# Kernel tuning notes

Hardware: AMD Instinct MI355X
Metric: run time of the kernel (lower is better)

Reference implementation:

```python
import jax, jax.numpy as jnp
import numpy as np

VOCAB, EMB, HID, SEQ, BATCH, LAYERS = 10000, 512, 1024, 128, 64, 2

def setup_inputs() -> dict:
    key = jax.random.key(0)
    ks = jax.random.split(key, 9)
    k_emb = np.sqrt(1.0 / HID)
    u = lambda k, shape, a: jax.random.uniform(k, shape, jnp.float32, -a, a)
    return {
        "inputs": jax.random.randint(ks[0], (SEQ, BATCH), 0, VOCAB),
        "hidden": jnp.zeros((LAYERS, BATCH, HID), jnp.float32),
        "emb": u(ks[1], (VOCAB, EMB), 0.1),
        "Wx0": u(ks[2], (HID, EMB), k_emb),
        "Wh0": u(ks[3], (HID, HID), k_emb),
        "bh0": u(ks[4], (HID,), k_emb),
        "Wx1": u(ks[5], (HID, HID), k_emb),
        "Wh1": u(ks[6], (HID, HID), k_emb),
        "bh1": u(ks[7], (HID,), k_emb),
        "Wout": u(ks[8], (VOCAB, HID), 0.1),
        "bout": u(jax.random.fold_in(key, 99), (VOCAB,), 0.1),
    }

def reference(inputs, hidden, emb, Wx0, Wh0, bh0, Wx1, Wh1, bh1, Wout, bout):
    # inputs: (S, B) int; hidden: (L, B, H). Dropout is identity (dp_keep_prob=1).
    embd = emb[inputs]  # (S, B, E)

    def step(h, x_t):
        h0 = jnp.tanh(x_t @ Wx0.T + h[0] @ Wh0.T + bh0)   # (B, H)
        h1 = jnp.tanh(h0 @ Wx1.T + h[1] @ Wh1.T + bh1)    # (B, H)
        logits_t = h1 @ Wout.T + bout                      # (B, V)
        return jnp.stack([h0, h1]), logits_t

    hidden_final, logits = jax.lax.scan(step, hidden, embd)
    return logits, hidden_final
```

## Files before the change

### kernel.cpp

```cpp
#include <hip/hip_runtime.h>
#include <hip/hip_bf16.h>


typedef unsigned short u16;
typedef unsigned int   u32;
typedef unsigned long long u64;
typedef __bf16 bf16x8 __attribute__((ext_vector_type(8)));
typedef float  f32x4  __attribute__((ext_vector_type(4)));

__device__ __forceinline__ u16 f2b(float f) {
  __hip_bfloat16 h = __float2bfloat16(f);
  return __builtin_bit_cast(u16, h);
}
__device__ __forceinline__ float b2f(u16 u) {
  return __bfloat162float(__builtin_bit_cast(__hip_bfloat16, u));
}

__device__ __forceinline__ void gload16(const void* g, void* lds) {
  __builtin_amdgcn_global_load_lds(
      (const __attribute__((address_space(1))) u32*)g,
      (__attribute__((address_space(3))) u32*)lds, 16, 0, 0);
}

__device__ __forceinline__ u64 aload64(const u64* p) {
  return __hip_atomic_load(p, __ATOMIC_RELAXED, __HIP_MEMORY_SCOPE_AGENT);
}
__device__ __forceinline__ void astore64(u64* p, u64 v) {
  __hip_atomic_store(p, v, __ATOMIC_RELAXED, __HIP_MEMORY_SCOPE_AGENT);
}
__device__ __forceinline__ int aloadi(const int* p) {
  return __hip_atomic_load(p, __ATOMIC_RELAXED, __HIP_MEMORY_SCOPE_AGENT);
}
__device__ __forceinline__ void astorei(int* p, int v) {
  __hip_atomic_store(p, v, __ATOMIC_RELAXED, __HIP_MEMORY_SCOPE_AGENT);
}
__device__ __forceinline__ int afetchadd(int* p) {
  return __hip_atomic_fetch_add(p, 1, __ATOMIC_RELAXED,
                                __HIP_MEMORY_SCOPE_AGENT);
}

__device__ __forceinline__ void stage16_1024(char* hbuf, const u64* src,
                                             int tid) {
  const int rsub = tid >> 8;
  const int coff = tid & 255;
  u64 tmp[4];
#pragma unroll
  for (int i = 0; i < 4; ++i) {
    int it = i * 4 + rsub;
    tmp[i] = aload64(src + it * 256 + coff);
  }
#pragma unroll
  for (int i = 0; i < 4; ++i) {
    int it = i * 4 + rsub;
    *(u64*)(hbuf + it * 2048 + ((coff * 8) ^ ((it & 7) << 4))) = tmp[i];
  }
}

__device__ __forceinline__ void cvt4(const float* __restrict__ s,
                                     u16* __restrict__ d, int n4,
                                     int gid, int stride) {
  for (int i = gid; i < n4; i += stride) {
    float4 f = ((const float4*)s)[i];
    ushort4 u;
    u.x = f2b(f.x); u.y = f2b(f.y); u.z = f2b(f.z); u.w = f2b(f.w);
    ((ushort4*)d)[i] = u;
  }
}

__global__ __launch_bounds__(256) void prep_kernel(
    const int* __restrict__ inputs, const float* __restrict__ hidden,
    const float* __restrict__ emb,
    const float* __restrict__ Wx0, const float* __restrict__ Wh0,
    const float* __restrict__ Wx1, const float* __restrict__ Wh1,
    const float* __restrict__ Wout,
    u16* Wx0b, u16* Wh0b, u16* Wcat1, u16* Woutb,
    u16* A0b, u16* Hh0, u16* Hh1, int* flags) {
  int gid = blockIdx.x * 256 + threadIdx.x;
  int stride = gridDim.x * 256;
  if (gid < 1024) flags[gid] = 0;
  cvt4(Wx0, Wx0b, 1024 * 512 / 4, gid, stride);
  cvt4(Wh0, Wh0b, 1024 * 1024 / 4, gid, stride);
  cvt4(Wout, Woutb, 10000 * 1024 / 4, gid, stride);
  cvt4(hidden, Hh0, 65536 / 4, gid, stride);
  cvt4(hidden + 65536, Hh1, 65536 / 4, gid, stride);
  for (int i = gid; i < 1024 * 512; i += stride) {
    int row = i >> 9, j = i & 511;
    float4 f = (j < 256) ? ((const float4*)Wx1)[row * 256 + j]
                         : ((const float4*)Wh1)[row * 256 + (j - 256)];
    ushort4 u;
    u.x = f2b(f.x); u.y = f2b(f.y); u.z = f2b(f.z); u.w = f2b(f.w);
    ((ushort4*)Wcat1)[i] = u;
  }
  for (int i = gid; i < 8192 * 128; i += stride) {
    int m = i >> 7, e4 = i & 127;
    int r = inputs[m];
    float4 f = ((const float4*)(emb + (size_t)r * 512))[e4];
    ushort4 u;
    u.x = f2b(f.x); u.y = f2b(f.y); u.z = f2b(f.z); u.w = f2b(f.w);
    ((ushort4*)A0b)[i] = u;
  }
}

__global__ __launch_bounds__(256) void gemm_bt(
    const u16* __restrict__ A, const u16* __restrict__ Bm,
    const float* __restrict__ bias, u16* __restrict__ Cout,
    int M, int N, int K) {
  const int tid = threadIdx.x;
  const int l = tid & 63;
  const int wv = tid >> 6;
  const int MT = M >> 7;
  const int bm = (int)blockIdx.x % MT;
  const int bn = (int)blockIdx.x / MT;
  const int m0 = bm * 128, n0 = bn * 128;

  __shared__ u16 As[128 * 32];
  __shared__ u16 Bs[128 * 32];

  const int fa0 = wv * 1024 + l * 16;
  const int fa1 = (4 + wv) * 1024 + l * 16;
  const int rowA0 = fa0 >> 6, kO0 = (fa0 & 63) >> 1;
  const int rowA1 = fa1 >> 6, kO1 = (fa1 & 63) >> 1;
  const u16* gA0 = A + (size_t)(m0 + rowA0) * K + kO0;
  const u16* gA1 = A + (size_t)(m0 + rowA1) * K + kO1;
  const u16* gB0 = Bm + (size_t)(n0 + rowA0) * K + kO0;
  const u16* gB1 = Bm + (size_t)(n0 + rowA1) * K + kO1;
  u16* lA0 = As + wv * 512;
  u16* lA1 = As + (4 + wv) * 512;
  u16* lB0 = Bs + wv * 512;
  u16* lB1 = Bs + (4 + wv) * 512;

  const int wm = wv >> 1, wn = wv & 1;
  const u16* pA = As + (wm * 64 + (l & 15)) * 32 + (l >> 4) * 8;
  const u16* pB = Bs + (wn * 64 + (l & 15)) * 32 + (l >> 4) * 8;

  f32x4 acc[4][4] = {};

  for (int k0 = 0; k0 < K; k0 += 32) {
    __syncthreads();
    gload16(gA0 + k0, lA0);
    gload16(gA1 + k0, lA1);
    gload16(gB0 + k0, lB0);
    gload16(gB1 + k0, lB1);
    asm volatile("s_waitcnt vmcnt(0)" ::: "memory");
    __syncthreads();
    bf16x8 a[4], b[4];
#pragma unroll
    for (int i = 0; i < 4; ++i) a[i] = *(const bf16x8*)(pA + i * 512);
#pragma unroll
    for (int j = 0; j < 4; ++j) b[j] = *(const bf16x8*)(pB + j * 512);
#pragma unroll
    for (int i = 0; i < 4; ++i)
#pragma unroll
      for (int j = 0; j < 4; ++j)
        acc[i][j] = __builtin_amdgcn_mfma_f32_16x16x32_bf16(a[i], b[j],
                                                            acc[i][j], 0, 0, 0);
  }

#pragma unroll
  for (int j = 0; j < 4; ++j) {
    int cn = n0 + wn * 64 + j * 16 + (l & 15);
    float bv = bias[cn];
#pragma unroll
    for (int i = 0; i < 4; ++i) {
      int rmb = m0 + wm * 64 + i * 16 + ((l >> 4) << 2);
#pragma unroll
      for (int r = 0; r < 4; ++r)
        Cout[(size_t)(rmb + r) * N + cn] = f2b(acc[i][j][r] + bv);
    }
  }
}

__global__ __launch_bounds__(1024, 4) void rnn_fused(
    const u16* __restrict__ X0, const u16* __restrict__ Wh0b,
    const u16* __restrict__ Wcat1, const float* __restrict__ bh1,
    u16* __restrict__ Hh0, u16* __restrict__ Hh1,
    const u16* __restrict__ Woutb, const float* __restrict__ bout,
    float* __restrict__ outL,
    float* __restrict__ hfin0, float* __restrict__ hfin1,
    int* __restrict__ flags) {
  __shared__ __align__(16) char smem[65664];
  const int tid = threadIdx.x;
  const int l = tid & 63;
  const int wv = tid >> 6;

  if (blockIdx.x < 32) {
    char* hbuf = smem;
    float (*red)[16][16] = (float(*)[16][16])(smem + 32768);
    u16* ht = (u16*)(smem + 40960);
    const int wg = (int)blockIdx.x;
    const int bg = wg & 3, cc = wg >> 2;
    const int cw = wv & 7, kw = wv >> 3;
    const int col = cc * 128 + cw * 16 + (l & 15);
    const int row = l & 15;
    const int sw = (row & 7) << 4;
    const int rowoff = row * 2048;
    const int kwbase = kw * 1024 + ((l >> 4) << 4);
    bf16x8 b[16];
    {
      const u16* wp = Wh0b + (size_t)col * 1024 + (kw * 512 + ((l >> 4) * 8));
#pragma unroll
      for (int kt = 0; kt < 16; ++kt) b[kt] = *(const bf16x8*)(wp + kt * 32);
    }
    int* cnt0 = flags + (bg << 4);
    int* done0 = flags + 64 + (bg << 4);

    for (int t = 0; t < 128; ++t) {
      float xv[4];
      if (kw == 0) {
#pragma unroll
        for (int r = 0; r < 4; ++r) {
          int bat = bg * 16 + (l >> 4) * 4 + r;
          xv[r] = b2f(X0[(size_t)(t * 64 + bat) * 1024 + col]);
        }
      }
      stage16_1024(hbuf, (const u64*)(Hh0 + ((size_t)t * 64 + bg * 16) * 1024),
                   tid);
      __syncthreads();
      f32x4 acc = {0.f, 0.f, 0.f, 0.f};
#pragma unroll
      for (int kt = 0; kt < 16; ++kt) {
        bf16x8 av =
            *(const bf16x8*)(hbuf + rowoff + ((kwbase + kt * 64) ^ sw));
        acc = __builtin_amdgcn_mfma_f32_16x16x32_bf16(av, b[kt], acc, 0, 0, 0);
      }
      if (kw == 1) {
#pragma unroll
        for (int r = 0; r < 4; ++r) red[cw][(l >> 4) * 4 + r][l & 15] = acc[r];
      }
      __syncthreads();
      if (kw == 0) {
#pragma unroll
        for (int r = 0; r < 4; ++r) {
          int br = (l >> 4) * 4 + r;
          float v = acc[r] + red[cw][br][l & 15] + xv[r];
          v = tanhf(v);
          ht[br * 128 + cw * 16 + (l & 15)] = f2b(v);
          if (t == 127) hfin0[(bg * 16 + br) * 1024 + col] = v;
        }
      }
      __syncthreads();
      if (tid < 512) {
        int rw = tid >> 5, seg = tid & 31;
        u64 v = ((const u64*)ht)[tid];
        u64* dp = (u64*)(Hh0 + ((size_t)(t + 1) * 64 + bg * 16 + rw) * 1024 +
                         cc * 128) + seg;
        astore64(dp, v);
      }
      asm volatile("s_waitcnt vmcnt(0)" ::: "memory");
      __syncthreads();
      if (tid == 0) {
        int old = afetchadd(cnt0);
        if (old == (t + 1) * 8 - 1) {
          astorei(done0, t + 1);
        } else if (t < 127) {
          while (aloadi(done0) < t + 1) __builtin_amdgcn_s_sleep(1);
        }
      }
      __syncthreads();
    }
  } else if (blockIdx.x < 96) {
    char* hbuf = smem;
    float (*red)[3][16][16] = (float(*)[3][16][16])(smem + 32768);
    u16* ht = (u16*)(smem + 45056);
    const int wg = (int)blockIdx.x - 32;
    const int bg = wg & 3, cc = wg >> 2;
    const int ch = wv & 3, kw = wv >> 2;
    const int col = cc * 64 + ch * 16 + (l & 15);
    const int row = l & 15;
    const int sw = (row & 7) << 4;
    const int rowoff = row * 2048;
    const int kwb = (kw & 1) * 1024 + ((l >> 4) << 4);
    bf16x8 b[16];
    {
      const u16* wp = Wcat1 + (size_t)col * 2048 + (kw * 512 + ((l >> 4) * 8));
#pragma unroll
      for (int kt = 0; kt < 16; ++kt) b[kt] = *(const bf16x8*)(wp + kt * 32);
    }
    const float bias = bh1[col];
    int* done0 = flags + 64 + (bg << 4);
    int* cnt1 = flags + 128 + (bg << 4);
    int* done1 = flags + 256 + (bg << 4);
    int* dlog = flags + 448 + (bg << 4);

    for (int s = 0; s < 128; ++s) {
      if (tid == 0) {
        while (aloadi(done0) < s + 1) __builtin_amdgcn_s_sleep(1);
      }
      __syncthreads();
      stage16_1024(hbuf,
                   (const u64*)(Hh0 + ((size_t)(s + 1) * 64 + bg * 16) * 1024),
                   tid);
      __syncthreads();
      f32x4 acc = {0.f, 0.f, 0.f, 0.f};
      if (kw < 2) {
#pragma unroll
        for (int kt = 0; kt < 16; ++kt) {
          bf16x8 av = *(const bf16x8*)(hbuf + rowoff + ((kwb + kt * 64) ^ sw));
          acc =
              __builtin_amdgcn_mfma_f32_16x16x32_bf16(av, b[kt], acc, 0, 0, 0);
        }
      }
      __syncthreads();
      if (tid == 0) {
        while (aloadi(done1) < s) __builtin_amdgcn_s_sleep(1);
      }
      __syncthreads();
      stage16_1024(hbuf, (const u64*)(Hh1 + ((size_t)s * 64 + bg * 16) * 1024),
                   tid);
      __syncthreads();
      if (kw >= 2) {
#pragma unroll
        for (int kt = 0; kt < 16; ++kt) {
          bf16x8 av = *(const bf16x8*)(hbuf + rowoff + ((kwb + kt * 64) ^ sw));
          acc =
              __builtin_amdgcn_mfma_f32_16x16x32_bf16(av, b[kt], acc, 0, 0, 0);
        }
      }
      if (kw != 0) {
#pragma unroll
        for (int r = 0; r < 4; ++r)
          red[ch][kw - 1][(l >> 4) * 4 + r][l & 15] = acc[r];
      }
      __syncthreads();
      if (kw == 0) {
#pragma unroll
        for (int r = 0; r < 4; ++r) {
          int br = (l >> 4) * 4 + r;
          int c = l & 15;
          float v = acc[r] + red[ch][0][br][c] + red[ch][1][br][c] +
                    red[ch][2][br][c] + bias;
          v = tanhf(v);
          ht[br * 64 + ch * 16 + c] = f2b(v);
          if (s == 127) hfin1[(bg * 16 + br) * 1024 + col] = v;
        }
      }
      __syncthreads();
      if (tid < 256) {
        int rw = tid >> 4, seg = tid & 15;
        u64 v = ((const u64*)ht)[tid];
        u64* dp = (u64*)(Hh1 + ((size_t)(s + 1) * 64 + bg * 16 + rw) * 1024 +
                         cc * 64) + seg;
        astore64(dp, v);
      }
      asm volatile("s_waitcnt vmcnt(0)" ::: "memory");
      __syncthreads();
      if (tid == 0) {
        int old = afetchadd(cnt1);
        if (old == (s + 1) * 16 - 1) {
          astorei(done1, s + 1);
          astorei(dlog, s + 1);
        }
      }
    }
  } else {
    const int sub = wv >> 2;
    const int wvl = wv & 3;
    u16* As = (u16*)(smem + sub * 16384);
    u16* Bs = (u16*)(smem + sub * 16384 + 8192);
    int* shid = (int*)(smem + 65600);
    const int cls = ((int)blockIdx.x - 96) & 7;
    const int sz = (79 - cls + 7) / 8;
    int* classq = flags + 640 + (cls << 4);
    int* dlg = flags + 448;

    const int fa0 = wvl * 1024 + l * 16;
    const int fa1 = (4 + wvl) * 1024 + l * 16;
    const int rowA0 = fa0 >> 6, kO0 = (fa0 & 63) >> 1;
    const int rowA1 = fa1 >> 6, kO1 = (fa1 & 63) >> 1;
    const u16* Abase = Hh1 + 65536;
    u16* lB0 = Bs + wvl * 512;
    u16* lB1 = Bs + (4 + wvl) * 512;
    u64* dA0 = (u64*)((char*)As + wvl * 1024 + l * 16);
    u64* dA1 = (u64*)((char*)As + (4 + wvl) * 1024 + l * 16);
    const int wm = wvl >> 1, wn = wvl & 1;
    const u16* pA = As + (wm * 64 + (l & 15)) * 32 + (l >> 4) * 8;
    const u16* pB = Bs + (wn * 64 + (l & 15)) * 32 + (l >> 4) * 8;

    for (;;) {
      if (tid == 0) *shid = afetchadd(classq);
      __syncthreads();
      const int base = *shid;
      __syncthreads();
      if (base >= 16 * sz) break;
      const int id = base * 4 + sub;
      const int u = id / sz, j = id - u * sz;
      const int nn = cls + j * 8;
      const int m0 = u * 128, n0 = nn * 128;

      if (tid == 0) {
        const int umax = (base * 4 + 3) / sz;
        const int tgt = 2 * umax + 2;
        for (;;) {
          int ok = 1;
#pragma unroll
          for (int g = 0; g < 4; ++g) ok &= (aloadi(dlg + g * 16) >= tgt);
          if (ok) break;
          __builtin_amdgcn_s_sleep(32);
        }
      }
      __syncthreads();

      const u16* gA0 = Abase + (size_t)(m0 + rowA0) * 1024 + kO0;
      const u16* gA1 = Abase + (size_t)(m0 + rowA1) * 1024 + kO1;
      int rB0 = n0 + rowA0; if (rB0 >= 10000) rB0 = 9999;
      int rB1 = n0 + rowA1; if (rB1 >= 10000) rB1 = 9999;
      const u16* gB0 = Woutb + (size_t)rB0 * 1024 + kO0;
      const u16* gB1 = Woutb + (size_t)rB1 * 1024 + kO1;

      f32x4 acc[4][4] = {};
      for (int k0 = 0; k0 < 1024; k0 += 32) {
        __syncthreads();
        const u64* pa0 = (const u64*)(gA0 + k0);
        const u64* pa1 = (const u64*)(gA1 + k0);
        u64 a00 = aload64(pa0), a01 = aload64(pa0 + 1);
        u64 a10 = aload64(pa1), a11 = aload64(pa1 + 1);
        gload16(gB0 + k0, lB0);
        gload16(gB1 + k0, lB1);
        dA0[0] = a00; dA0[1] = a01;
        dA1[0] = a10; dA1[1] = a11;
        asm volatile("s_waitcnt vmcnt(0)" ::: "memory");
        __syncthreads();
        bf16x8 a[4], b[4];
#pragma unroll
        for (int i = 0; i < 4; ++i) a[i] = *(const bf16x8*)(pA + i * 512);
#pragma unroll
        for (int j2 = 0; j2 < 4; ++j2) b[j2] = *(const bf16x8*)(pB + j2 * 512);
#pragma unroll
        for (int i = 0; i < 4; ++i)
#pragma unroll
          for (int j2 = 0; j2 < 4; ++j2)
            acc[i][j2] = __builtin_amdgcn_mfma_f32_16x16x32_bf16(
                a[i], b[j2], acc[i][j2], 0, 0, 0);
      }
#pragma unroll
      for (int j2 = 0; j2 < 4; ++j2) {
        int cn = n0 + wn * 64 + j2 * 16 + (l & 15);
        if (cn >= 10000) continue;
        float bv = bout[cn];
#pragma unroll
        for (int i = 0; i < 4; ++i) {
          int rmb = m0 + wm * 64 + i * 16 + ((l >> 4) << 2);
#pragma unroll
          for (int r = 0; r < 4; ++r)
            outL[(size_t)(rmb + r) * 10000 + cn] = acc[i][j2][r] + bv;
        }
      }
    }
  }
}

extern "C" void kernel_launch(void* const* d_in, const int* in_sizes, int n_in,
                              void* d_out, int out_size, void* d_ws,
                              size_t ws_size, hipStream_t stream) {
  const int*   inputs = (const int*)d_in[0];
  const float* hidden = (const float*)d_in[1];
  const float* emb    = (const float*)d_in[2];
  const float* Wx0    = (const float*)d_in[3];
  const float* Wh0    = (const float*)d_in[4];
  const float* bh0    = (const float*)d_in[5];
  const float* Wx1    = (const float*)d_in[6];
  const float* Wh1    = (const float*)d_in[7];
  const float* bh1    = (const float*)d_in[8];
  const float* Wout   = (const float*)d_in[9];
  const float* bout   = (const float*)d_in[10];
  float* out = (float*)d_out;

  if (ws_size < (size_t)88 * 1024 * 1024) return;

  char* w = (char*)d_ws;
  u16* Wx0b  = (u16*)w; w += 1048576;
  u16* Wh0b  = (u16*)w; w += 2097152;
  u16* Wcat1 = (u16*)w; w += 4194304;
  u16* Woutb = (u16*)w; w += 20480000;
  u16* A0b   = (u16*)w; w += 8388608;
  u16* X0b   = (u16*)w; w += 16777216;
  u16* Hh0   = (u16*)w; w += 16908288;
  u16* Hh1   = (u16*)w; w += 16908288;
  int* flags = (int*)w;

  float* hfin0 = out + 81920000;
  float* hfin1 = out + 81920000 + 65536;

  prep_kernel<<<2048, 256, 0, stream>>>(inputs, hidden, emb, Wx0, Wh0, Wx1,
                                        Wh1, Wout, Wx0b, Wh0b, Wcat1, Woutb,
                                        A0b, Hh0, Hh1, flags);
  gemm_bt<<<512, 256, 0, stream>>>(A0b, Wx0b, bh0, X0b, 8192, 1024, 512);
  rnn_fused<<<256, 1024, 0, stream>>>(X0b, Wh0b, Wcat1, bh1, Hh0, Hh1, Woutb,
                                      bout, out, hfin0, hfin1, flags);
}
```

Before: 669.0 us.

## Co-locate recurrent blocks per XCD and use plain cached loads when same-XCD

Recurrent blocks are remapped by blockIdx mod 8 so that each batch group's blocks are likely placed on one XCD. At start they exchange their XCC_ID through flags to check this. When all 24 blocks of a group share an XCD, the per-step hidden-state exchange uses ordinary loads and stores through the shared L2 instead of agent-scope atomics. A second local copy of Hh1 serves the recurrent readers, while the global copy stays for the output GEMM on other XCDs. The change relies on the hardware's round-robin block placement, and correctness of the fast path depends on L2 coherence within one XCD.

Measured after the change: 1.280 ms. 1.91x slower.

```diff
diff --git a/kernel.cpp b/kernel.cpp
--- a/kernel.cpp
+++ b/kernel.cpp
@@ -40,14 +40,22 @@
 }
 
 __device__ __forceinline__ void stage16_1024(char* hbuf, const u64* src,
-                                             int tid) {
+                                             int tid, int fast) {
   const int rsub = tid >> 8;
   const int coff = tid & 255;
   u64 tmp[4];
-#pragma unroll
-  for (int i = 0; i < 4; ++i) {
-    int it = i * 4 + rsub;
-    tmp[i] = aload64(src + it * 256 + coff);
+  if (fast) {
+#pragma unroll
+    for (int i = 0; i < 4; ++i) {
+      int it = i * 4 + rsub;
+      tmp[i] = src[it * 256 + coff];
+    }
+  } else {
+#pragma unroll
+    for (int i = 0; i < 4; ++i) {
+      int it = i * 4 + rsub;
+      tmp[i] = aload64(src + it * 256 + coff);
+    }
   }
 #pragma unroll
   for (int i = 0; i < 4; ++i) {
@@ -74,7 +82,7 @@
     const float* __restrict__ Wx1, const float* __restrict__ Wh1,
     const float* __restrict__ Wout,
     u16* Wx0b, u16* Wh0b, u16* Wcat1, u16* Woutb,
-    u16* A0b, u16* Hh0, u16* Hh1, int* flags) {
+    u16* A0b, u16* Hh0, u16* Hh1L, u16* Hh1G, int* flags) {
   int gid = blockIdx.x * 256 + threadIdx.x;
   int stride = gridDim.x * 256;
   if (gid < 1024) flags[gid] = 0;
@@ -82,7 +90,8 @@
   cvt4(Wh0, Wh0b, 1024 * 1024 / 4, gid, stride);
   cvt4(Wout, Woutb, 10000 * 1024 / 4, gid, stride);
   cvt4(hidden, Hh0, 65536 / 4, gid, stride);
-  cvt4(hidden + 65536, Hh1, 65536 / 4, gid, stride);
+  cvt4(hidden + 65536, Hh1L, 65536 / 4, gid, stride);
+  cvt4(hidden + 65536, Hh1G, 65536 / 4, gid, stride);
   for (int i = gid; i < 1024 * 512; i += stride) {
     int row = i >> 9, j = i & 511;
     float4 f = (j < 256) ? ((const float4*)Wx1)[row * 256 + j]
@@ -173,7 +182,7 @@
 __global__ __launch_bounds__(1024, 4) void rnn_fused(
     const u16* __restrict__ X0, const u16* __restrict__ Wh0b,
     const u16* __restrict__ Wcat1, const float* __restrict__ bh1,
-    u16* __restrict__ Hh0, u16* __restrict__ Hh1,
+    u16* __restrict__ Hh0, u16* __restrict__ Hh1L, u16* __restrict__ Hh1G,
     const u16* __restrict__ Woutb, const float* __restrict__ bout,
     float* __restrict__ outL,
     float* __restrict__ hfin0, float* __restrict__ hfin1,
@@ -182,13 +191,38 @@
   const int tid = threadIdx.x;
   const int l = tid & 63;
   const int wv = tid >> 6;
-
-  if (blockIdx.x < 32) {
+  const int r = (int)blockIdx.x & 7;
+  const int k = (int)blockIdx.x >> 3;
+  const bool isRec = (r < 4) && (k < 24);
+
+  int fastf = 0;
+  if (isRec) {
+    int xcc;
+    asm volatile("s_getreg_b32 %0, hwreg(HW_REG_XCC_ID)" : "=s"(xcc));
+    int* xt = flags + 768 + r * 32;
+    if (tid == 0) astorei(xt + k, xcc + 1);
+    int* sflag = (int*)smem;
+    if (tid < 24) {
+      int v;
+      while ((v = aloadi(xt + tid)) == 0) __builtin_amdgcn_s_sleep(1);
+      sflag[tid] = (v == xcc + 1);
+    }
+    __syncthreads();
+    if (tid == 0) {
+      int f = 1;
+      for (int i = 0; i < 24; ++i) f &= sflag[i];
+      sflag[32] = f;
+    }
+    __syncthreads();
+    fastf = sflag[32];
+    __syncthreads();
+  }
+
+  if (isRec && k < 8) {
     char* hbuf = smem;
     float (*red)[16][16] = (float(*)[16][16])(smem + 32768);
     u16* ht = (u16*)(smem + 40960);
-    const int wg = (int)blockIdx.x;
-    const int bg = wg & 3, cc = wg >> 2;
+    const int bg = r, cc = k;
     const int cw = wv & 7, kw = wv >> 3;
     const int col = cc * 128 + cw * 16 + (l & 15);
     const int row = l & 15;
@@ -208,13 +242,13 @@
       float xv[4];
       if (kw == 0) {
 #pragma unroll
-        for (int r = 0; r < 4; ++r) {
-          int bat = bg * 16 + (l >> 4) * 4 + r;
-          xv[r] = b2f(X0[(size_t)(t * 64 + bat) * 1024 + col]);
+        for (int q = 0; q < 4; ++q) {
+          int bat = bg * 16 + (l >> 4) * 4 + q;
+          xv[q] = b2f(X0[(size_t)(t * 64 + bat) * 1024 + col]);
         }
       }
       stage16_1024(hbuf, (const u64*)(Hh0 + ((size_t)t * 64 + bg * 16) * 1024),
-                   tid);
+                   tid, fastf);
       __syncthreads();
       f32x4 acc = {0.f, 0.f, 0.f, 0.f};
 #pragma unroll
@@ -225,14 +259,14 @@
       }
       if (kw == 1) {
 #pragma unroll
-        for (int r = 0; r < 4; ++r) red[cw][(l >> 4) * 4 + r][l & 15] = acc[r];
+        for (int q = 0; q < 4; ++q) red[cw][(l >> 4) * 4 + q][l & 15] = acc[q];
       }
       __syncthreads();
       if (kw == 0) {
 #pragma unroll
-        for (int r = 0; r < 4; ++r) {
-          int br = (l >> 4) * 4 + r;
-          float v = acc[r] + red[cw][br][l & 15] + xv[r];
+        for (int q = 0; q < 4; ++q) {
+          int br = (l >> 4) * 4 + q;
+          float v = acc[q] + red[cw][br][l & 15] + xv[q];
           v = tanhf(v);
           ht[br * 128 + cw * 16 + (l & 15)] = f2b(v);
           if (t == 127) hfin0[(bg * 16 + br) * 1024 + col] = v;
@@ -244,7 +278,7 @@
         u64 v = ((const u64*)ht)[tid];
         u64* dp = (u64*)(Hh0 + ((size_t)(t + 1) * 64 + bg * 16 + rw) * 1024 +
                          cc * 128) + seg;
-        astore64(dp, v);
+        if (fastf) *dp = v; else astore64(dp, v);
       }
       asm volatile("s_waitcnt vmcnt(0)" ::: "memory");
       __syncthreads();
@@ -258,12 +292,11 @@
       }
       __syncthreads();
     }
-  } else if (blockIdx.x < 96) {
+  } else if (isRec) {
     char* hbuf = smem;
     float (*red)[3][16][16] = (float(*)[3][16][16])(smem + 32768);
     u16* ht = (u16*)(smem + 45056);
-    const int wg = (int)blockIdx.x - 32;
-    const int bg = wg & 3, cc = wg >> 2;
+    const int bg = r, cc = k - 8;
     const int ch = wv & 3, kw = wv >> 2;
     const int col = cc * 64 + ch * 16 + (l & 15);
     const int row = l & 15;
@@ -281,6 +314,7 @@
     int* cnt1 = flags + 128 + (bg << 4);
     int* done1 = flags + 256 + (bg << 4);
     int* dlog = flags + 448 + (bg << 4);
+    const u16* Hh1rd = fastf ? Hh1L : Hh1G;
 
     for (int s = 0; s < 128; ++s) {
       if (tid == 0) {
@@ -289,7 +323,7 @@
       __syncthreads();
       stage16_1024(hbuf,
                    (const u64*)(Hh0 + ((size_t)(s + 1) * 64 + bg * 16) * 1024),
-                   tid);
+                   tid, fastf);
       __syncthreads();
       f32x4 acc = {0.f, 0.f, 0.f, 0.f};
       if (kw < 2) {
@@ -305,8 +339,9 @@
         while (aloadi(done1) < s) __builtin_amdgcn_s_sleep(1);
       }
       __syncthreads();
-      stage16_1024(hbuf, (const u64*)(Hh1 + ((size_t)s * 64 + bg * 16) * 1024),
-                   tid);
+      stage16_1024(hbuf,
+                   (const u64*)(Hh1rd + ((size_t)s * 64 + bg * 16) * 1024),
+                   tid, fastf);
       __syncthreads();
       if (kw >= 2) {
 #pragma unroll
@@ -318,16 +353,16 @@
       }
       if (kw != 0) {
 #pragma unroll
-        for (int r = 0; r < 4; ++r)
-          red[ch][kw - 1][(l >> 4) * 4 + r][l & 15] = acc[r];
+        for (int q = 0; q < 4; ++q)
+          red[ch][kw - 1][(l >> 4) * 4 + q][l & 15] = acc[q];
       }
       __syncthreads();
       if (kw == 0) {
 #pragma unroll
-        for (int r = 0; r < 4; ++r) {
-          int br = (l >> 4) * 4 + r;
+        for (int q = 0; q < 4; ++q) {
+          int br = (l >> 4) * 4 + q;
           int c = l & 15;
-          float v = acc[r] + red[ch][0][br][c] + red[ch][1][br][c] +
+          float v = acc[q] + red[ch][0][br][c] + red[ch][1][br][c] +
                     red[ch][2][br][c] + bias;
           v = tanhf(v);
           ht[br * 64 + ch * 16 + c] = f2b(v);
@@ -338,9 +373,9 @@
       if (tid < 256) {
         int rw = tid >> 4, seg = tid & 15;
         u64 v = ((const u64*)ht)[tid];
-        u64* dp = (u64*)(Hh1 + ((size_t)(s + 1) * 64 + bg * 16 + rw) * 1024 +
-                         cc * 64) + seg;
-        astore64(dp, v);
+        size_t off = ((size_t)(s + 1) * 64 + bg * 16 + rw) * 1024 + cc * 64;
+        astore64((u64*)(Hh1G + off) + seg, v);
+        if (fastf) *((u64*)(Hh1L + off) + seg) = v;
       }
       asm volatile("s_waitcnt vmcnt(0)" ::: "memory");
       __syncthreads();
@@ -358,7 +393,7 @@
     u16* As = (u16*)(smem + sub * 16384);
     u16* Bs = (u16*)(smem + sub * 16384 + 8192);
     int* shid = (int*)(smem + 65600);
-    const int cls = ((int)blockIdx.x - 96) & 7;
+    const int cls = r;
     const int sz = (79 - cls + 7) / 8;
     int* classq = flags + 640 + (cls << 4);
     int* dlg = flags + 448;
@@ -367,7 +402,7 @@
     const int fa1 = (4 + wvl) * 1024 + l * 16;
     const int rowA0 = fa0 >> 6, kO0 = (fa0 & 63) >> 1;
     const int rowA1 = fa1 >> 6, kO1 = (fa1 & 63) >> 1;
-    const u16* Abase = Hh1 + 65536;
+    const u16* Abase = Hh1G + 65536;
     u16* lB0 = Bs + wvl * 512;
     u16* lB1 = Bs + (4 + wvl) * 512;
     u64* dA0 = (u64*)((char*)As + wvl * 1024 + l * 16);
@@ -441,8 +476,8 @@
         for (int i = 0; i < 4; ++i) {
           int rmb = m0 + wm * 64 + i * 16 + ((l >> 4) << 2);
 #pragma unroll
-          for (int r = 0; r < 4; ++r)
-            outL[(size_t)(rmb + r) * 10000 + cn] = acc[i][j2][r] + bv;
+          for (int q = 0; q < 4; ++q)
+            outL[(size_t)(rmb + q) * 10000 + cn] = acc[i][j2][q] + bv;
         }
       }
     }
@@ -465,7 +500,7 @@
   const float* bout   = (const float*)d_in[10];
   float* out = (float*)d_out;
 
-  if (ws_size < (size_t)88 * 1024 * 1024) return;
+  if (ws_size < (size_t)100 * 1024 * 1024) return;
 
   char* w = (char*)d_ws;
   u16* Wx0b  = (u16*)w; w += 1048576;
@@ -475,7 +510,8 @@
   u16* A0b   = (u16*)w; w += 8388608;
   u16* X0b   = (u16*)w; w += 16777216;
   u16* Hh0   = (u16*)w; w += 16908288;
-  u16* Hh1   = (u16*)w; w += 16908288;
+  u16* Hh1L  = (u16*)w; w += 16908288;
+  u16* Hh1G  = (u16*)w; w += 16908288;
   int* flags = (int*)w;
 
   float* hfin0 = out + 81920000;
@@ -483,8 +519,8 @@
 
   prep_kernel<<<2048, 256, 0, stream>>>(inputs, hidden, emb, Wx0, Wh0, Wx1,
                                         Wh1, Wout, Wx0b, Wh0b, Wcat1, Woutb,
-                                        A0b, Hh0, Hh1, flags);
+                                        A0b, Hh0, Hh1L, Hh1G, flags);
   gemm_bt<<<512, 256, 0, stream>>>(A0b, Wx0b, bh0, X0b, 8192, 1024, 512);
-  rnn_fused<<<256, 1024, 0, stream>>>(X0b, Wh0b, Wcat1, bh1, Hh0, Hh1, Woutb,
-                                      bout, out, hfin0, hfin1, flags);
-}
+  rnn_fused<<<256, 1024, 0, stream>>>(X0b, Wh0b, Wcat1, bh1, Hh0, Hh1L, Hh1G,
+                                      Woutb, bout, out, hfin0, hfin1, flags);
+}
```
